# Kernel tuning notes

Hardware: AMD Instinct MI355X
Metric: run time of the kernel (lower is better)

The kernel has to match this reference:

```python
import jax, jax.numpy as jnp
import numpy as np

B, L, C = 4, 4096, 64

def setup_inputs() -> dict:
    key = jax.random.key(0)
    ks = jax.random.split(key, 7)
    s = 1.0 / np.sqrt(C)
    return {
        "x": jax.random.normal(ks[0], (B, L, C), dtype=jnp.float32),
        "Wq": jax.random.normal(ks[1], (C, C), dtype=jnp.float32) * s,
        "bq": jnp.zeros((C,), dtype=jnp.float32),
        "Wk": jax.random.normal(ks[2], (C, C), dtype=jnp.float32) * s,
        "bk": jnp.zeros((C,), dtype=jnp.float32),
        "Wv": jax.random.normal(ks[3], (C, C), dtype=jnp.float32) * s,
        "bv": jnp.zeros((C,), dtype=jnp.float32),
    }

def reference(x, Wq, bq, Wk, bk, Wv, bv):
    # Conv1D kernel_size=1 == pointwise linear over channels
    Q = jnp.einsum('blc,cf->blf', x, Wq) + bq  # [B, L, F]
    K = jnp.einsum('blc,cf->blf', x, Wk) + bk
    V = jnp.einsum('blc,cf->blf', x, Wv) + bv
    F = Wq.shape[1]
    scores = jnp.einsum('bqf,bkf->bqk', Q, K) / jnp.sqrt(jnp.float32(F))  # [B, Lq, Lk]
    # NOTE: original uses tf.keras.layers.Softmax(axis=1) -> normalize over QUERY axis
    attn = jax.nn.softmax(scores, axis=1)
    out = jnp.einsum('bqk,bkf->bqf', attn, V)
    return out + x
```

## Files before the change

kernel.cpp:

```cpp
#include <hip/hip_runtime.h>
#include <math.h>


#define BB 4
#define LL 4096
#define CC 64
#define C2 0.18033688011112042f

typedef __attribute__((ext_vector_type(8)))  short bf16x8;
typedef __attribute__((ext_vector_type(4)))  float f32x4;
typedef __attribute__((ext_vector_type(16))) float f32x16;
typedef __attribute__((ext_vector_type(4)))  unsigned int u32x4;

#define MFMA16(a, b, c) __builtin_amdgcn_mfma_f32_16x16x32_bf16(a, b, c, 0, 0, 0)
#define MFMA32(a, b, c) __builtin_amdgcn_mfma_f32_32x32x16_bf16(a, b, c, 0, 0, 0)
#define EXP2(x) __builtin_amdgcn_exp2f(x)

#define GLD4(dst, voff, base, imm) \
    asm volatile("global_load_dwordx4 %0, %1, %2 offset:%c3" \
                 : "=v"(dst) : "v"(voff), "s"(base), "i"(imm))
#define WAITVM0() asm volatile("s_waitcnt vmcnt(0)" ::: "memory")
#define PRIO(n) __builtin_amdgcn_s_setprio(n)

static __device__ __forceinline__ bf16x8 asbf(u32x4 v) {
    union { u32x4 a; bf16x8 b; } u; u.a = v; return u.b;
}
static __device__ __forceinline__ unsigned short f2bf(float f) {
    union { float f; unsigned u; } v; v.f = f;
    unsigned r = v.u + 0x7FFFu + ((v.u >> 16) & 1u);
    return (unsigned short)(r >> 16);
}
static __device__ __forceinline__ float bf2f(unsigned short h) {
    union { unsigned u; float f; } v; v.u = ((unsigned)h) << 16; return v.f;
}
static __device__ __forceinline__ bf16x8 pack8(float4 a, float4 b) {
    bf16x8 r;
    r[0] = (short)f2bf(a.x); r[1] = (short)f2bf(a.y);
    r[2] = (short)f2bf(a.z); r[3] = (short)f2bf(a.w);
    r[4] = (short)f2bf(b.x); r[5] = (short)f2bf(b.y);
    r[6] = (short)f2bf(b.z); r[7] = (short)f2bf(b.w);
    return r;
}
static __device__ __forceinline__ unsigned cvtpk(float lo, float hi) {
    unsigned r;
    asm("v_cvt_pk_bf16_f32 %0, %1, %2" : "=v"(r) : "v"(lo), "v"(hi));
    return r;
}
static __device__ __forceinline__ bf16x8 lds_frag(const unsigned short* p) {
    union { uint2 u[2]; bf16x8 b; } t;
    t.u[0] = *(const uint2*)(p);
    t.u[1] = *(const uint2*)(p + 4);
    return t.b;
}
static __device__ __forceinline__ void lds_put(unsigned short* p, u32x4 v) {
    *(uint2*)(p)     = make_uint2(v[0], v[1]);
    *(uint2*)(p + 4) = make_uint2(v[2], v[3]);
}

__global__ __launch_bounds__(512) void k_qkv(
    const float* __restrict__ x,
    const float* __restrict__ Wq, const float* __restrict__ bq,
    const float* __restrict__ Wk, const float* __restrict__ bk,
    const float* __restrict__ Wv, const float* __restrict__ bv,
    unsigned short* __restrict__ Qb, unsigned short* __restrict__ Kb,
    unsigned short* __restrict__ Vt)
{
    __shared__ float Wl[64 * 64];
    __shared__ unsigned short ldsV[64 * 72];
    const int bid = blockIdx.x;
    const int mat = bid % 3;
    const int r0 = (bid / 3) * 64;
    const int tid = threadIdx.x, w = tid >> 6, lane = tid & 63;
    const int c = lane & 15, g = lane >> 4;
    const int rw = (w >> 1) * 16;
    const int c0 = (w & 1) * 32;

    const float* W  = (mat == 0) ? Wq : (mat == 1) ? Wk : Wv;
    const float* bs = (mat == 0) ? bq : (mat == 1) ? bk : bv;

    {
        const float4* wsrc = (const float4*)W;
        float4* wdst = (float4*)Wl;
        wdst[tid] = wsrc[tid];
        wdst[tid + 512] = wsrc[tid + 512];
    }

    const float* xr = x + (size_t)(r0 + rw + c) * CC;
    const bf16x8 ax0 = pack8(((const float4*)xr)[2 * g], ((const float4*)xr)[2 * g + 1]);
    const bf16x8 ax1 = pack8(((const float4*)xr)[8 + 2 * g], ((const float4*)xr)[8 + 2 * g + 1]);
    __syncthreads();

    f32x4 acc0 = {0.f, 0.f, 0.f, 0.f}, acc1 = {0.f, 0.f, 0.f, 0.f};
    {
        const int col = c0 + c;
        bf16x8 b0, b1;
        #pragma unroll
        for (int j = 0; j < 8; ++j) {
            b0[j] = (short)f2bf(Wl[(8 * g + j) * 64 + col]);
            b1[j] = (short)f2bf(Wl[(32 + 8 * g + j) * 64 + col]);
        }
        acc0 = MFMA16(ax0, b0, acc0); acc0 = MFMA16(ax1, b1, acc0);
    }
    {
        const int col = c0 + 16 + c;
        bf16x8 b0, b1;
        #pragma unroll
        for (int j = 0; j < 8; ++j) {
            b0[j] = (short)f2bf(Wl[(8 * g + j) * 64 + col]);
            b1[j] = (short)f2bf(Wl[(32 + 8 * g + j) * 64 + col]);
        }
        acc1 = MFMA16(ax0, b0, acc1); acc1 = MFMA16(ax1, b1, acc1);
    }
    const float bias0 = bs[c0 + c], bias1 = bs[c0 + 16 + c];

    if (mat < 2) {
        unsigned short* dst = (mat == 0) ? Qb : Kb;
        #pragma unroll
        for (int r = 0; r < 4; ++r) {
            const size_t row = (size_t)(r0 + rw + 4 * g + r) * CC;
            dst[row + c0 + c]      = f2bf(acc0[r] + bias0);
            dst[row + c0 + 16 + c] = f2bf(acc1[r] + bias1);
        }
    } else {
        #pragma unroll
        for (int r = 0; r < 4; ++r) {
            const int rowin = rw + 4 * g + r;
            ldsV[(c0 + c) * 72 + rowin]      = f2bf(acc0[r] + bias0);
            ldsV[(c0 + 16 + c) * 72 + rowin] = f2bf(acc1[r] + bias1);
        }
        __syncthreads();
        const int b = r0 >> 12, kt = (r0 & 4095) >> 6;
        const int f = tid >> 3, jj = tid & 7;
        *(uint4*)(Vt + (((size_t)(b * 64 + kt) * 64 + f) * 64) + jj * 8) =
            *(const uint4*)(ldsV + f * 72 + jj * 8);
    }
}

__global__ __launch_bounds__(512, 4) void k_stats(
    const unsigned short* __restrict__ Qb, const unsigned short* __restrict__ Kb,
    unsigned short* __restrict__ Vt)
{
    const int nb = ((blockIdx.x & 7) << 6) | (blockIdx.x >> 3);
    const int b = nb >> 7, kt32 = nb & 127;
    const int kbase = kt32 * 32;
    const int tid = threadIdx.x, w = tid >> 6, lane = tid & 63;
    const int l31 = lane & 31, hi = lane >> 5;

    __shared__ unsigned short qsm[256 * 68];
    __shared__ float pl[8][32];
    __shared__ float rls[32];

    const unsigned short* kr = Kb + ((size_t)b * LL + kbase + l31) * CC + 8 * hi;
    const bf16x8 ak0 = *(const bf16x8*)(kr);
    const bf16x8 ak1 = *(const bf16x8*)(kr + 16);
    const bf16x8 ak2 = *(const bf16x8*)(kr + 32);
    const bf16x8 ak3 = *(const bf16x8*)(kr + 48);

    const unsigned short* const sQ = Qb + (size_t)b * LL * CC;
    const unsigned gbase = (unsigned)((((tid >> 3) * 64) + (tid & 7) * 8) * 2);
    const int woff = (tid >> 3) * 68 + (tid & 7) * 8;
    const unsigned short* const Qt = qsm + (w * 32 + l31) * 68 + 8 * hi;

    u32x4 S0, S1, S2, S3;
    #define QISS(s_) do { \
        const unsigned vo = gbase + (unsigned)(s_) * 32768u; \
        GLD4(S0, vo, sQ, 0); GLD4(S1, vo + 8192u, sQ, 0); \
        GLD4(S2, vo + 16384u, sQ, 0); GLD4(S3, vo + 24576u, sQ, 0); \
    } while (0)

    QISS(0);
    f32x16 lacc = {};
    for (int s = 0; s < 16; ++s) {
        WAITVM0();
        __syncthreads();
        lds_put(qsm + woff,         S0);
        lds_put(qsm + woff + 4352,  S1);
        lds_put(qsm + woff + 8704,  S2);
        lds_put(qsm + woff + 13056, S3);
        __syncthreads();
        if (s < 15) QISS(s + 1);
        const bf16x8 q0 = lds_frag(Qt);
        const bf16x8 q1 = lds_frag(Qt + 16);
        const bf16x8 q2 = lds_frag(Qt + 32);
        const bf16x8 q3 = lds_frag(Qt + 48);
        f32x16 T = {};
        PRIO(1);
        T = MFMA32(ak0, q0, T); T = MFMA32(ak1, q1, T);
        T = MFMA32(ak2, q2, T); T = MFMA32(ak3, q3, T);
        PRIO(0);
        #pragma unroll
        for (int r = 0; r < 16; ++r) lacc[r] += EXP2(T[r] * C2);
    }
    #undef QISS

    #pragma unroll
    for (int r = 0; r < 16; ++r) {
        float v = lacc[r];
        v += __shfl_xor(v, 1);  v += __shfl_xor(v, 2);
        v += __shfl_xor(v, 4);  v += __shfl_xor(v, 8);
        v += __shfl_xor(v, 16);
        lacc[r] = v;
    }
    if (l31 == 0) {
        #pragma unroll
        for (int r = 0; r < 16; ++r)
            pl[w][(r & 3) + 8 * (r >> 2) + 4 * hi] = lacc[r];
    }
    __syncthreads();
    if (tid < 32) {
        float L = 0.f;
        #pragma unroll
        for (int ww = 0; ww < 8; ++ww) L += pl[ww][tid];
        rls[tid] = 1.0f / L;
    }
    __syncthreads();

    {
        const int ktv = kt32 >> 1, kin0 = (kt32 & 1) * 32;
        const int f = tid >> 3, j = tid & 7;
        unsigned short* vp = Vt + (((size_t)(b * 64 + ktv) * 64 + f) * 64) + kin0 + j * 4;
        ushort4 v = *(const ushort4*)vp;
        v.x = f2bf(bf2f(v.x) * rls[j * 4 + 0]);
        v.y = f2bf(bf2f(v.y) * rls[j * 4 + 1]);
        v.z = f2bf(bf2f(v.z) * rls[j * 4 + 2]);
        v.w = f2bf(bf2f(v.w) * rls[j * 4 + 3]);
        *(ushort4*)vp = v;
    }
}

__global__ __launch_bounds__(512, 4) void k_out(
    const float* __restrict__ x,
    const unsigned short* __restrict__ Qb, const unsigned short* __restrict__ Kb,
    const unsigned short* __restrict__ Vt,
    float* __restrict__ out)
{
    const int nb = ((blockIdx.x & 7) << 6) | (blockIdx.x >> 3);
    const int b = nb >> 7, qt = nb & 127;
    const int q0 = qt * 32;
    const int tid = threadIdx.x, w = tid >> 6, lane = tid & 63;
    const int l31 = lane & 31, hi = lane >> 5;

    __shared__ unsigned short smem[256 * 68 + 64 * 260];
    unsigned short* const KT = smem;
    unsigned short* const VT = smem + 256 * 68;

    const unsigned short* qr = Qb + ((size_t)b * LL + q0 + l31) * CC + 8 * hi;
    const bf16x8 qb0 = *(const bf16x8*)(qr);
    const bf16x8 qb1 = *(const bf16x8*)(qr + 16);
    const bf16x8 qb2 = *(const bf16x8*)(qr + 32);
    const bf16x8 qb3 = *(const bf16x8*)(qr + 48);

    const unsigned short* const sK = Kb + (size_t)b * LL * CC;
    const unsigned short* const sV = Vt + (size_t)b * 64 * 64 * 64;
    const unsigned gbase = (unsigned)((((tid >> 3) * 64) + (tid & 7) * 8) * 2);
    const int wK = (tid >> 3) * 68 + (tid & 7) * 8;
    const int wV = (tid >> 3) * 260 + (tid & 7) * 8;
    const unsigned short* const Ka = KT + (w * 32 + l31) * 68 + 8 * hi;
    const unsigned short* const Va = VT + l31 * 260 + w * 32 + 8 * hi;
    const unsigned short* const Vb2 = VT + (l31 + 32) * 260 + w * 32 + 8 * hi;

    u32x4 S0, S1, S2, S3, S4, S5, S6, S7;
    #define STG(s_) do { \
        const unsigned vo = gbase + (unsigned)(s_) * 32768u; \
        GLD4(S0, vo, sK, 0); GLD4(S1, vo + 8192u, sK, 0); \
        GLD4(S2, vo + 16384u, sK, 0); GLD4(S3, vo + 24576u, sK, 0); \
        GLD4(S4, vo, sV, 0); GLD4(S5, vo + 8192u, sV, 0); \
        GLD4(S6, vo + 16384u, sV, 0); GLD4(S7, vo + 24576u, sV, 0); \
    } while (0)

    STG(0);
    f32x16 oacc0 = {}, oacc1 = {};

    for (int s = 0; s < 16; ++s) {
        WAITVM0();
        __syncthreads();
        lds_put(KT + wK,         S0);
        lds_put(KT + wK + 4352,  S1);
        lds_put(KT + wK + 8704,  S2);
        lds_put(KT + wK + 13056, S3);
        lds_put(VT + wV,       S4);
        lds_put(VT + wV + 64,  S5);
        lds_put(VT + wV + 128, S6);
        lds_put(VT + wV + 192, S7);
        __syncthreads();
        if (s < 15) STG(s + 1);
        const bf16x8 ak0 = lds_frag(Ka);
        const bf16x8 ak1 = lds_frag(Ka + 16);
        const bf16x8 ak2 = lds_frag(Ka + 32);
        const bf16x8 ak3 = lds_frag(Ka + 48);
        f32x16 T = {};
        PRIO(1);
        T = MFMA32(ak0, qb0, T); T = MFMA32(ak1, qb1, T);
        T = MFMA32(ak2, qb2, T); T = MFMA32(ak3, qb3, T);
        PRIO(0);
        unsigned u0 = cvtpk(EXP2(T[0] * C2),  EXP2(T[1] * C2));
        unsigned u1 = cvtpk(EXP2(T[2] * C2),  EXP2(T[3] * C2));
        unsigned u2 = cvtpk(EXP2(T[4] * C2),  EXP2(T[5] * C2));
        unsigned u3 = cvtpk(EXP2(T[6] * C2),  EXP2(T[7] * C2));
        unsigned u4 = cvtpk(EXP2(T[8] * C2),  EXP2(T[9] * C2));
        unsigned u5 = cvtpk(EXP2(T[10] * C2), EXP2(T[11] * C2));
        unsigned u6 = cvtpk(EXP2(T[12] * C2), EXP2(T[13] * C2));
        unsigned u7 = cvtpk(EXP2(T[14] * C2), EXP2(T[15] * C2));
        asm volatile("s_nop 1");
        asm("v_permlane32_swap_b32 %0, %1" : "+v"(u0), "+v"(u2));
        asm("v_permlane32_swap_b32 %0, %1" : "+v"(u1), "+v"(u3));
        asm("v_permlane32_swap_b32 %0, %1" : "+v"(u4), "+v"(u6));
        asm("v_permlane32_swap_b32 %0, %1" : "+v"(u5), "+v"(u7));
        u32x4 f1, f2;
        f1[0] = u0; f1[1] = u1; f1[2] = u2; f1[3] = u3;
        f2[0] = u4; f2[1] = u5; f2[2] = u6; f2[3] = u7;
        const bf16x8 v00 = lds_frag(Va);
        const bf16x8 v01 = lds_frag(Va + 16);
        const bf16x8 v10 = lds_frag(Vb2);
        const bf16x8 v11 = lds_frag(Vb2 + 16);
        PRIO(1);
        oacc0 = MFMA32(v00, asbf(f1), oacc0);
        oacc0 = MFMA32(v01, asbf(f2), oacc0);
        oacc1 = MFMA32(v10, asbf(f1), oacc1);
        oacc1 = MFMA32(v11, asbf(f2), oacc1);
        PRIO(0);
    }
    #undef STG

    __syncthreads();
    float* ocomb = (float*)smem;
    for (int i = tid; i < 32 * 68; i += 512) ocomb[i] = 0.f;
    __syncthreads();
    #pragma unroll
    for (int r = 0; r < 16; ++r) {
        const int fr = (r & 3) + 8 * (r >> 2) + 4 * hi;
        atomicAdd(&ocomb[l31 * 68 + fr],      oacc0[r]);
        atomicAdd(&ocomb[l31 * 68 + 32 + fr], oacc1[r]);
    }
    __syncthreads();
    {
        const int q = tid >> 4, fc = tid & 15;
        const size_t row = (size_t)b * LL + q0 + q;
        const float4 xv = ((const float4*)(x + row * CC))[fc];
        const float4 ov = *(const float4*)(&ocomb[q * 68 + fc * 4]);
        ((float4*)(out + row * CC))[fc] =
            make_float4(xv.x + ov.x, xv.y + ov.y, xv.z + ov.z, xv.w + ov.w);
    }
}

extern "C" void kernel_launch(void* const* d_in, const int* in_sizes, int n_in,
                              void* d_out, int out_size, void* d_ws, size_t ws_size,
                              hipStream_t stream)
{
    const float* x  = (const float*)d_in[0];
    const float* Wq = (const float*)d_in[1];
    const float* bq = (const float*)d_in[2];
    const float* Wk = (const float*)d_in[3];
    const float* bk = (const float*)d_in[4];
    const float* Wv = (const float*)d_in[5];
    const float* bv = (const float*)d_in[6];
    float* out = (float*)d_out;

    const size_t n = (size_t)BB * LL * CC;
    unsigned short* Qb = (unsigned short*)d_ws;
    unsigned short* Kb = Qb + n;
    unsigned short* Vt = Kb + n;

    hipLaunchKernelGGL(k_qkv, dim3(3 * BB * LL / 64), dim3(512), 0, stream,
                       x, Wq, bq, Wk, bk, Wv, bv, Qb, Kb, Vt);
    hipLaunchKernelGGL(k_stats, dim3(BB * (LL / 32)), dim3(512), 0, stream,
                       Qb, Kb, Vt);
    hipLaunchKernelGGL(k_out, dim3(BB * (LL / 32)), dim3(512), 0, stream,
                       x, Qb, Kb, Vt, out);
}
```

Before: 109.4 us.

## Give each wave private double-buffered K/Q/V LDS tiles and drop block barriers

```diff
diff --git a/kernel.cpp b/kernel.cpp
--- a/kernel.cpp
+++ b/kernel.cpp
@@ -20,6 +20,7 @@
     asm volatile("global_load_dwordx4 %0, %1, %2 offset:%c3" \
                  : "=v"(dst) : "v"(voff), "s"(base), "i"(imm))
 #define WAITVM0() asm volatile("s_waitcnt vmcnt(0)" ::: "memory")
+#define SBAR() __builtin_amdgcn_sched_barrier(0)
 #define PRIO(n) __builtin_amdgcn_s_setprio(n)
 
 static __device__ __forceinline__ bf16x8 asbf(u32x4 v) {
@@ -129,10 +130,10 @@
             ldsV[(c0 + 16 + c) * 72 + rowin] = f2bf(acc1[r] + bias1);
         }
         __syncthreads();
-        const int b = r0 >> 12, kt = (r0 & 4095) >> 6;
-        const int f = tid >> 3, jj = tid & 7;
-        *(uint4*)(Vt + (((size_t)(b * 64 + kt) * 64 + f) * 64) + jj * 8) =
-            *(const uint4*)(ldsV + f * 72 + jj * 8);
+        const int b = r0 >> 12, ktb = (r0 & 4095) >> 5;
+        const int h = tid >> 8, f = (tid >> 2) & 63, ch = tid & 3;
+        *(uint4*)(Vt + ((size_t)(b * 128 + ktb + h) * 64 + f) * 32 + ch * 8)
+            = *(const uint4*)(ldsV + f * 72 + h * 32 + ch * 8);
     }
 }
 
@@ -146,7 +147,7 @@
     const int tid = threadIdx.x, w = tid >> 6, lane = tid & 63;
     const int l31 = lane & 31, hi = lane >> 5;
 
-    __shared__ unsigned short qsm[256 * 68];
+    __shared__ unsigned short qsm[8][2][32 * 68];
     __shared__ float pl[8][32];
     __shared__ float rls[32];
 
@@ -157,41 +158,47 @@
     const bf16x8 ak3 = *(const bf16x8*)(kr + 48);
 
     const unsigned short* const sQ = Qb + (size_t)b * LL * CC;
-    const unsigned gbase = (unsigned)((((tid >> 3) * 64) + (tid & 7) * 8) * 2);
-    const int woff = (tid >> 3) * 68 + (tid & 7) * 8;
-    const unsigned short* const Qt = qsm + (w * 32 + l31) * 68 + 8 * hi;
+    const unsigned wqoff = (unsigned)(w * 65536);
+    const int wb = (lane >> 3) * 68 + (lane & 7) * 8;
+    unsigned short* const q0b = &qsm[w][0][0];
+    unsigned short* const q1b = &qsm[w][1][0];
 
     u32x4 S0, S1, S2, S3;
     #define QISS(s_) do { \
-        const unsigned vo = gbase + (unsigned)(s_) * 32768u; \
-        GLD4(S0, vo, sQ, 0); GLD4(S1, vo + 8192u, sQ, 0); \
-        GLD4(S2, vo + 16384u, sQ, 0); GLD4(S3, vo + 24576u, sQ, 0); \
-    } while (0)
-
-    QISS(0);
+        const unsigned vo = wqoff + (unsigned)((s_) * 4096 + lane * 16); \
+        GLD4(S0, vo, sQ, 0);    GLD4(S1, vo, sQ, 1024); \
+        GLD4(S2, vo, sQ, 2048); GLD4(S3, vo, sQ, 3072); \
+    } while (0)
+    #define QWR(dst) do { \
+        unsigned short* _p = (dst) + wb; \
+        lds_put(_p, S0);        lds_put(_p + 544, S1); \
+        lds_put(_p + 1088, S2); lds_put(_p + 1632, S3); \
+    } while (0)
+
+    QISS(0); WAITVM0(); SBAR(); QWR(q0b); QISS(1);
+
     f32x16 lacc = {};
     for (int s = 0; s < 16; ++s) {
-        WAITVM0();
-        __syncthreads();
-        lds_put(qsm + woff,         S0);
-        lds_put(qsm + woff + 4352,  S1);
-        lds_put(qsm + woff + 8704,  S2);
-        lds_put(qsm + woff + 13056, S3);
-        __syncthreads();
-        if (s < 15) QISS(s + 1);
-        const bf16x8 q0 = lds_frag(Qt);
-        const bf16x8 q1 = lds_frag(Qt + 16);
-        const bf16x8 q2 = lds_frag(Qt + 32);
-        const bf16x8 q3 = lds_frag(Qt + 48);
+        const unsigned short* qp = ((s & 1) ? q1b : q0b) + l31 * 68 + hi * 8;
+        const bf16x8 b0 = lds_frag(qp);
+        const bf16x8 b1 = lds_frag(qp + 16);
+        const bf16x8 b2 = lds_frag(qp + 32);
+        const bf16x8 b3 = lds_frag(qp + 48);
         f32x16 T = {};
         PRIO(1);
-        T = MFMA32(ak0, q0, T); T = MFMA32(ak1, q1, T);
-        T = MFMA32(ak2, q2, T); T = MFMA32(ak3, q3, T);
+        T = MFMA32(ak0, b0, T); T = MFMA32(ak1, b1, T);
+        T = MFMA32(ak2, b2, T); T = MFMA32(ak3, b3, T);
         PRIO(0);
         #pragma unroll
         for (int r = 0; r < 16; ++r) lacc[r] += EXP2(T[r] * C2);
+        if (s < 15) {
+            WAITVM0(); SBAR();
+            QWR((s & 1) ? q0b : q1b);
+            if (s < 14) QISS(s + 2);
+        }
     }
     #undef QISS
+    #undef QWR
 
     #pragma unroll
     for (int r = 0; r < 16; ++r) {
@@ -216,19 +223,18 @@
     __syncthreads();
 
     {
-        const int ktv = kt32 >> 1, kin0 = (kt32 & 1) * 32;
-        const int f = tid >> 3, j = tid & 7;
-        unsigned short* vp = Vt + (((size_t)(b * 64 + ktv) * 64 + f) * 64) + kin0 + j * 4;
-        ushort4 v = *(const ushort4*)vp;
-        v.x = f2bf(bf2f(v.x) * rls[j * 4 + 0]);
-        v.y = f2bf(bf2f(v.y) * rls[j * 4 + 1]);
-        v.z = f2bf(bf2f(v.z) * rls[j * 4 + 2]);
-        v.w = f2bf(bf2f(v.w) * rls[j * 4 + 3]);
-        *(ushort4*)vp = v;
-    }
-}
-
-__global__ __launch_bounds__(512, 4) void k_out(
+        unsigned short* vbase = Vt + ((size_t)(b * 128 + kt32)) * 2048;
+        const int kin0 = (tid & 7) * 4;
+        ushort4 v = *(const ushort4*)(vbase + tid * 4);
+        v.x = f2bf(bf2f(v.x) * rls[kin0 + 0]);
+        v.y = f2bf(bf2f(v.y) * rls[kin0 + 1]);
+        v.z = f2bf(bf2f(v.z) * rls[kin0 + 2]);
+        v.w = f2bf(bf2f(v.w) * rls[kin0 + 3]);
+        *(ushort4*)(vbase + tid * 4) = v;
+    }
+}
+
+__global__ __launch_bounds__(512, 2) void k_out(
     const float* __restrict__ x,
     const unsigned short* __restrict__ Qb, const unsigned short* __restrict__ Kb,
     const unsigned short* __restrict__ Vt,
@@ -240,9 +246,8 @@
     const int tid = threadIdx.x, w = tid >> 6, lane = tid & 63;
     const int l31 = lane & 31, hi = lane >> 5;
 
-    __shared__ unsigned short smem[256 * 68 + 64 * 260];
-    unsigned short* const KT = smem;
-    unsigned short* const VT = smem + 256 * 68;
+    __shared__ unsigned short ksm[8][2][32 * 68];
+    __shared__ unsigned short vsm[8][2][64 * 36];
 
     const unsigned short* qr = Qb + ((size_t)b * LL + q0 + l31) * CC + 8 * hi;
     const bf16x8 qb0 = *(const bf16x8*)(qr);
@@ -251,47 +256,52 @@
     const bf16x8 qb3 = *(const bf16x8*)(qr + 48);
 
     const unsigned short* const sK = Kb + (size_t)b * LL * CC;
-    const unsigned short* const sV = Vt + (size_t)b * 64 * 64 * 64;
-    const unsigned gbase = (unsigned)((((tid >> 3) * 64) + (tid & 7) * 8) * 2);
-    const int wK = (tid >> 3) * 68 + (tid & 7) * 8;
-    const int wV = (tid >> 3) * 260 + (tid & 7) * 8;
-    const unsigned short* const Ka = KT + (w * 32 + l31) * 68 + 8 * hi;
-    const unsigned short* const Va = VT + l31 * 260 + w * 32 + 8 * hi;
-    const unsigned short* const Vb2 = VT + (l31 + 32) * 260 + w * 32 + 8 * hi;
-
-    u32x4 S0, S1, S2, S3, S4, S5, S6, S7;
-    #define STG(s_) do { \
-        const unsigned vo = gbase + (unsigned)(s_) * 32768u; \
-        GLD4(S0, vo, sK, 0); GLD4(S1, vo + 8192u, sK, 0); \
-        GLD4(S2, vo + 16384u, sK, 0); GLD4(S3, vo + 24576u, sK, 0); \
-        GLD4(S4, vo, sV, 0); GLD4(S5, vo + 8192u, sV, 0); \
-        GLD4(S6, vo + 16384u, sV, 0); GLD4(S7, vo + 24576u, sV, 0); \
-    } while (0)
-
-    STG(0);
+    const unsigned short* const sV = Vt + (size_t)b * 128 * 2048;
+    const unsigned wkoff = (unsigned)(w * 65536);
+    const unsigned wvoff = (unsigned)(w * 65536);
+    const int kwb = (lane >> 3) * 68 + (lane & 7) * 8;
+    const int vwb = (lane >> 2) * 36 + (lane & 3) * 8;
+
+    u32x4 K0, K1, K2, K3, V0, V1, V2, V3;
+    #define KISS(s_) do { \
+        const unsigned vo = wkoff + (unsigned)((s_) * 4096 + lane * 16); \
+        GLD4(K0, vo, sK, 0);    GLD4(K1, vo, sK, 1024); \
+        GLD4(K2, vo, sK, 2048); GLD4(K3, vo, sK, 3072); \
+    } while (0)
+    #define VISS(s_) do { \
+        const unsigned vo = wvoff + (unsigned)((s_) * 4096 + lane * 16); \
+        GLD4(V0, vo, sV, 0);    GLD4(V1, vo, sV, 1024); \
+        GLD4(V2, vo, sV, 2048); GLD4(V3, vo, sV, 3072); \
+    } while (0)
+    #define KWR(dst) do { \
+        unsigned short* _p = (dst) + kwb; \
+        lds_put(_p, K0);        lds_put(_p + 544, K1); \
+        lds_put(_p + 1088, K2); lds_put(_p + 1632, K3); \
+    } while (0)
+    #define VWR(dst) do { \
+        unsigned short* _p = (dst) + vwb; \
+        lds_put(_p, V0);        lds_put(_p + 576, V1); \
+        lds_put(_p + 1152, V2); lds_put(_p + 1728, V3); \
+    } while (0)
+
+    KISS(0); VISS(0); WAITVM0(); SBAR();
+    KWR(&ksm[w][0][0]); VWR(&vsm[w][0][0]);
+    KISS(1); VISS(1);
+
     f32x16 oacc0 = {}, oacc1 = {};
 
     for (int s = 0; s < 16; ++s) {
-        WAITVM0();
-        __syncthreads();
-        lds_put(KT + wK,         S0);
-        lds_put(KT + wK + 4352,  S1);
-        lds_put(KT + wK + 8704,  S2);
-        lds_put(KT + wK + 13056, S3);
-        lds_put(VT + wV,       S4);
-        lds_put(VT + wV + 64,  S5);
-        lds_put(VT + wV + 128, S6);
-        lds_put(VT + wV + 192, S7);
-        __syncthreads();
-        if (s < 15) STG(s + 1);
-        const bf16x8 ak0 = lds_frag(Ka);
-        const bf16x8 ak1 = lds_frag(Ka + 16);
-        const bf16x8 ak2 = lds_frag(Ka + 32);
-        const bf16x8 ak3 = lds_frag(Ka + 48);
+        const unsigned short* Kt = &ksm[w][s & 1][0];
+        const unsigned short* Vl = &vsm[w][s & 1][0];
+        const unsigned short* kp = Kt + l31 * 68 + hi * 8;
+        const bf16x8 a0 = lds_frag(kp);
+        const bf16x8 a1 = lds_frag(kp + 16);
+        const bf16x8 a2 = lds_frag(kp + 32);
+        const bf16x8 a3 = lds_frag(kp + 48);
         f32x16 T = {};
         PRIO(1);
-        T = MFMA32(ak0, qb0, T); T = MFMA32(ak1, qb1, T);
-        T = MFMA32(ak2, qb2, T); T = MFMA32(ak3, qb3, T);
+        T = MFMA32(a0, qb0, T); T = MFMA32(a1, qb1, T);
+        T = MFMA32(a2, qb2, T); T = MFMA32(a3, qb3, T);
         PRIO(0);
         unsigned u0 = cvtpk(EXP2(T[0] * C2),  EXP2(T[1] * C2));
         unsigned u1 = cvtpk(EXP2(T[2] * C2),  EXP2(T[3] * C2));
@@ -309,21 +319,32 @@
         u32x4 f1, f2;
         f1[0] = u0; f1[1] = u1; f1[2] = u2; f1[3] = u3;
         f2[0] = u4; f2[1] = u5; f2[2] = u6; f2[3] = u7;
-        const bf16x8 v00 = lds_frag(Va);
-        const bf16x8 v01 = lds_frag(Va + 16);
-        const bf16x8 v10 = lds_frag(Vb2);
-        const bf16x8 v11 = lds_frag(Vb2 + 16);
+        const unsigned short* vp0 = Vl + l31 * 36 + hi * 8;
+        const unsigned short* vp1 = Vl + (32 + l31) * 36 + hi * 8;
+        const bf16x8 v00 = lds_frag(vp0);
+        const bf16x8 v01 = lds_frag(vp0 + 16);
+        const bf16x8 v10 = lds_frag(vp1);
+        const bf16x8 v11 = lds_frag(vp1 + 16);
         PRIO(1);
         oacc0 = MFMA32(v00, asbf(f1), oacc0);
         oacc0 = MFMA32(v01, asbf(f2), oacc0);
         oacc1 = MFMA32(v10, asbf(f1), oacc1);
         oacc1 = MFMA32(v11, asbf(f2), oacc1);
         PRIO(0);
-    }
-    #undef STG
-
-    __syncthreads();
-    float* ocomb = (float*)smem;
+        if (s < 15) {
+            WAITVM0(); SBAR();
+            KWR(&ksm[w][(s + 1) & 1][0]);
+            VWR(&vsm[w][(s + 1) & 1][0]);
+            if (s < 14) { KISS(s + 2); VISS(s + 2); }
+        }
+    }
+    #undef KISS
+    #undef VISS
+    #undef KWR
+    #undef VWR
+
+    __syncthreads();
+    float* ocomb = (float*)&ksm[0][0][0];
     for (int i = tid; i < 32 * 68; i += 512) ocomb[i] = 0.f;
     __syncthreads();
     #pragma unroll
```

Measured after the change: 104.4 us. 4.6% less time.
